# Optimization experiments

Measured on AMD Instinct MI355X. Metric: run time of the kernel, lower is better.

Reference implementation:

```python
import jax, jax.numpy as jnp
import numpy as np

LEN = 2048
DIM = 1024
DFF = 4096  # dim * dim_ff_scale
EPS = 1e-5


def layer_norm(x, g, b):
    mu = jnp.mean(x, axis=-1, keepdims=True)
    var = jnp.mean((x - mu) ** 2, axis=-1, keepdims=True)
    return (x - mu) * jax.lax.rsqrt(var + EPS) * g + b


def ffn(x, w1, b1, w2, b2):
    h = jax.nn.silu(x @ w1 + b1)
    return h @ w2 + b2


def setup_inputs() -> dict:
    key = jax.random.key(0)
    ks = jax.random.split(key, 16)
    s1 = 1.0 / np.sqrt(DIM)
    s2 = 1.0 / np.sqrt(DFF)
    return {
        "z": jax.random.normal(ks[0], (8, LEN, DIM), jnp.float32),
        "pos": jax.random.normal(ks[1], (LEN, DIM), jnp.float32),
        "a": jax.random.normal(ks[2], (1,), jnp.float32),
        "hidden_init": jax.random.normal(ks[3], (LEN, DIM), jnp.float32),
        "ln_g": jnp.ones((DIM,), jnp.float32),
        "ln_b": jnp.zeros((DIM,), jnp.float32),
        "wp1": jax.random.uniform(ks[4], (DIM, DFF), jnp.float32, -s1, s1),
        "bp1": jax.random.uniform(ks[5], (DFF,), jnp.float32, -s1, s1),
        "wp2": jax.random.uniform(ks[6], (DFF, DIM), jnp.float32, -s2, s2),
        "bp2": jax.random.uniform(ks[7], (DIM,), jnp.float32, -s2, s2),
        "w1": jax.random.uniform(ks[8], (DIM, DFF), jnp.float32, -s1, s1),
        "b1": jax.random.uniform(ks[9], (DFF,), jnp.float32, -s1, s1),
        "w2": jax.random.uniform(ks[10], (DFF, DIM), jnp.float32, -s2, s2),
        "b2": jax.random.uniform(ks[11], (DIM,), jnp.float32, -s2, s2),
    }


def reference(z, pos, a, hidden_init, ln_g, ln_b, wp1, bp1, wp2, bp2, w1, b1, w2, b2):
    # hidden starts as hidden_init broadcast to batch; it is detached in torch
    hidden = jax.lax.stop_gradient(jnp.broadcast_to(hidden_init[None], z.shape))
    # FFT of layer-normed input, zero-padded to 2*LEN along time axis
    fz = jnp.fft.rfft(layer_norm(z, ln_g, ln_b), n=2 * LEN, axis=1)  # [B, LEN+1, D] complex
    # implicit filter: FFN over positional encodings, windowed by exp decay
    h = ffn(pos, wp1, bp1, wp2, bp2)  # [LEN, D]
    window = jnp.exp(-jnp.arange(LEN, dtype=z.dtype) * jnp.exp(a[0]))  # [LEN]
    wfh = jnp.fft.rfft(window[:, None] * h, n=2 * LEN, axis=0)  # [LEN+1, D]
    z_hidden = jnp.fft.irfft(wfh[None] * fz, axis=1)  # [B, 2*LEN, D]
    znew = z_hidden[:, :LEN] + hidden
    out = ffn(layer_norm(znew, ln_g, ln_b), w1, b1, w2, b2) + znew
    return out
```

## Files before the change

kernel.cpp:

```cpp
#include <hip/hip_runtime.h>


typedef unsigned short u16;
typedef unsigned int u32;
typedef __attribute__((ext_vector_type(8))) short short8;
typedef __attribute__((ext_vector_type(4))) float f32x4;

#define DEVINL __device__ __forceinline__

constexpr size_t MiB = 1ull << 20;
constexpr size_t WS_BYTES = 256 * MiB;
__device__ __attribute__((aligned(256))) char g_ws[WS_BYTES];

constexpr size_t OFF_BUF0  = 0;
constexpr size_t OFF_ZNEW  = 64 * MiB;
constexpr size_t OFF_A1    = 128 * MiB;
constexpr size_t OFF_HB    = 160 * MiB;
constexpr size_t OFF_WFH   = 176 * MiB;
constexpr size_t OFF_POSB  = 193 * MiB;
constexpr size_t OFF_WP1T  = 197 * MiB;
constexpr size_t OFF_WP2T  = 205 * MiB;
constexpr size_t OFF_W1T   = 213 * MiB;
constexpr size_t OFF_W2T   = 221 * MiB;
constexpr size_t OFF_WFILT = 229 * MiB;
constexpr size_t OFF_HIDT  = 237 * MiB;
constexpr size_t OFF_MEAN  = 245 * MiB;
constexpr size_t OFF_RSTD  = 245 * MiB + 65536;

DEVINL u16 f2b(float x) {
  u32 u = __builtin_bit_cast(u32, x);
  return (u16)((u + 0x7fffu + ((u >> 16) & 1u)) >> 16);
}
DEVINL float b2f(u16 h) { u32 u = ((u32)h) << 16; return __builtin_bit_cast(float, u); }
DEVINL float silu_f(float x) { return x / (1.f + __expf(-x)); }

DEVINL void gll16(const u16* g, u16* l) {
  __builtin_amdgcn_global_load_lds((const __attribute__((address_space(1))) u32*)(const void*)g,
                                   (__attribute__((address_space(3))) u32*)(void*)l, 16, 0, 0);
}


__global__ __launch_bounds__(256) void conv_bf16(const float* __restrict__ in,
                                                 u16* __restrict__ o) {
  int i = (blockIdx.x * 256 + threadIdx.x) * 4;
  float4 v = *(const float4*)&in[i];
  o[i + 0] = f2b(v.x); o[i + 1] = f2b(v.y); o[i + 2] = f2b(v.z); o[i + 3] = f2b(v.w);
}

template<int OM>
__global__ __launch_bounds__(256) void transpose_prep(const float* __restrict__ in, int R, int C,
                                                      u16* __restrict__ oh, float* __restrict__ of) {
  __shared__ float tl[64][65];
  int c0 = blockIdx.x * 64, r0 = blockIdx.y * 64;
  int tx = threadIdx.x & 63, ty = threadIdx.x >> 6;
#pragma unroll
  for (int i = 0; i < 16; ++i) {
    int r = ty + i * 4;
    tl[r][tx] = in[(size_t)(r0 + r) * C + c0 + tx];
  }
  __syncthreads();
#pragma unroll
  for (int i = 0; i < 16; ++i) {
    int c = ty + i * 4;
    float v = tl[tx][c];
    size_t o = (size_t)(c0 + c) * R + r0 + tx;
    if constexpr (OM == 1) oh[o] = f2b(v);
    else of[o] = v;
  }
}


__global__ __launch_bounds__(256) void ln_transpose(const float* __restrict__ z,
                                                    const float* __restrict__ g,
                                                    const float* __restrict__ bb,
                                                    float* __restrict__ xnT) {
  int tid = threadIdx.x;
  int b = blockIdx.y, t0 = blockIdx.x * 8;
  __shared__ float tile[8 * 1024];
  __shared__ float smu[8], srs[8], ps[8][4], pq[8][4];
  const float* zp = z + ((size_t)b * 2048 + (size_t)t0) * 1024;
  float s[8], q[8];
#pragma unroll
  for (int r = 0; r < 8; ++r) {
    float4 v = *(const float4*)&zp[r * 1024 + tid * 4];
    *(float4*)&tile[r * 1024 + tid * 4] = v;
    s[r] = v.x + v.y + v.z + v.w;
    q[r] = v.x * v.x + v.y * v.y + v.z * v.z + v.w * v.w;
  }
  int ln = tid & 63, wv = tid >> 6;
#pragma unroll
  for (int r = 0; r < 8; ++r) {
#pragma unroll
    for (int off = 32; off; off >>= 1) { s[r] += __shfl_down(s[r], off); q[r] += __shfl_down(q[r], off); }
    if (ln == 0) { ps[r][wv] = s[r]; pq[r][wv] = q[r]; }
  }
  __syncthreads();
  if (tid < 8) {
    float ss = ps[tid][0] + ps[tid][1] + ps[tid][2] + ps[tid][3];
    float qq = pq[tid][0] + pq[tid][1] + pq[tid][2] + pq[tid][3];
    float mu = ss * (1.f / 1024.f);
    smu[tid] = mu;
    srs[tid] = rsqrtf(qq * (1.f / 1024.f) - mu * mu + 1e-5f);
  }
  __syncthreads();
#pragma unroll
  for (int rep = 0; rep < 4; ++rep) {
    int d = rep * 256 + tid;
    float gg = g[d], b2 = bb[d];
    float o[8];
#pragma unroll
    for (int t = 0; t < 8; ++t) o[t] = (tile[t * 1024 + d] - smu[t]) * srs[t] * gg + b2;
    float* op = xnT + (size_t)b * 2097152 + (size_t)d * 2048 + t0;
    *(float4*)&op[0] = make_float4(o[0], o[1], o[2], o[3]);
    *(float4*)&op[4] = make_float4(o[4], o[5], o[6], o[7]);
  }
}

template<int BM, int BN, int MODE>
__global__ __launch_bounds__(256) void gemm_bt(
    const u16* __restrict__ A, const u16* __restrict__ B,
    int N, int K,
    const float* __restrict__ bias, const float* __restrict__ resid,
    const float* __restrict__ a_scalar,
    float* __restrict__ outF, u16* __restrict__ outH) {
  constexpr int FM = BM / 32, FN = BN / 32;
  constexpr int TA = BM * 64, TB = BN * 64;
  __shared__ __align__(16) u16 sm[TA + TB];
  u16* sA = sm;
  u16* sB = sm + TA;

  const int tid = threadIdx.x;
  const int lane = tid & 63;
  const int wv = tid >> 6;
  const int wr = wv >> 1, wc = wv & 1;
  const int fr = lane & 15, fq = lane >> 4;
  const int mBase = blockIdx.y * BM;
  const int nBase = blockIdx.x * BN;

  f32x4 acc[FM][FN];
#pragma unroll
  for (int i = 0; i < FM; ++i)
#pragma unroll
    for (int j = 0; j < FN; ++j) acc[i][j] = (f32x4){0.f, 0.f, 0.f, 0.f};

#pragma unroll 1
  for (int k0 = 0; k0 < K; k0 += 64) {
#pragma unroll
    for (int it = 0; it < BM / 32; ++it) {
      int lin = it * 256 + tid, r = lin >> 3, c = (lin & 7) << 3;
      gll16(A + (size_t)(mBase + r) * K + k0 + c, sA + lin * 8);
    }
#pragma unroll
    for (int it = 0; it < BN / 32; ++it) {
      int lin = it * 256 + tid, r = lin >> 3, c = (lin & 7) << 3;
      gll16(B + (size_t)(nBase + r) * K + k0 + c, sB + lin * 8);
    }
    __syncthreads();
#pragma unroll
    for (int kk = 0; kk < 2; ++kk) {
      short8 af[FM], bf[FN];
#pragma unroll
      for (int i = 0; i < FM; ++i)
        af[i] = *(const short8*)&sA[(wr * (BM / 2) + i * 16 + fr) * 64 + kk * 32 + fq * 8];
#pragma unroll
      for (int j = 0; j < FN; ++j)
        bf[j] = *(const short8*)&sB[(wc * (BN / 2) + j * 16 + fr) * 64 + kk * 32 + fq * 8];
#pragma unroll
      for (int i = 0; i < FM; ++i)
#pragma unroll
        for (int j = 0; j < FN; ++j)
          acc[i][j] = __builtin_amdgcn_mfma_f32_16x16x32_bf16(af[i], bf[j], acc[i][j], 0, 0, 0);
    }
    __syncthreads();
  }

  float ea = 0.f;
  if constexpr (MODE == 1) ea = __expf(a_scalar[0]);
#pragma unroll
  for (int i = 0; i < FM; ++i)
#pragma unroll
    for (int j = 0; j < FN; ++j)
#pragma unroll
      for (int r = 0; r < 4; ++r) {
        int gr = mBase + wr * (BM / 2) + i * 16 + fq * 4 + r;
        int gc = nBase + wc * (BN / 2) + j * 16 + fr;
        size_t o = (size_t)gr * (size_t)N + (size_t)gc;
        float x = acc[i][j][r];
        if constexpr (MODE == 0) {
          outH[o] = f2b(silu_f(x + bias[gc]));
        } else if constexpr (MODE == 1) {
          x += bias[gr];
          x *= __expf(-(float)gc * ea);
          outF[o] = x;
        } else {
          outF[o] = x + bias[gc] + resid[o];
        }
      }
}

template<int SIGN>
DEVINL void fft4096(float2* x, float2* y, int tid) {
  float c0 = ((float)SIGN) * (6.283185307179586f / 4096.f);
#pragma unroll 1
  for (int st = 0; st < 12; ++st) {
#pragma unroll
    for (int vv = 0; vv < 8; ++vv) {
      int u = vv * 256 + tid;
      int p = u >> st;
      float2 a = x[u];
      float2 b = x[u + 2048];
      float ang = c0 * (float)p;
      float sn, cs;
      __sincosf(ang, &sn, &cs);
      float mx = a.x - b.x, my = a.y - b.y;
      int base = u + (p << st);
      y[base] = make_float2(a.x + b.x, a.y + b.y);
      y[base + (1 << st)] = make_float2(mx * cs - my * sn, mx * sn + my * cs);
    }
    __syncthreads();
    float2* t = x; x = y; y = t;
    c0 *= 2.f;
  }
}

__global__ __launch_bounds__(256) void fft_filter(const float* __restrict__ wfilt,
                                                  float2* __restrict__ wfh) {
  __shared__ float2 bufA[4096], bufB[4096];
  int tid = threadIdx.x, pr = blockIdx.x;
  int d0 = 2 * pr, d1 = d0 + 1;
  const float* u = wfilt + (size_t)d0 * 2048;
  const float* v = u + 2048;
#pragma unroll
  for (int j = 0; j < 16; ++j) {
    int idx = j * 256 + tid;
    bufA[idx] = (idx < 2048) ? make_float2(u[idx], v[idx]) : make_float2(0.f, 0.f);
  }
  __syncthreads();
  fft4096<-1>(bufA, bufB, tid);
  float2* o0 = wfh + (size_t)d0 * 2049;
  float2* o1 = wfh + (size_t)d1 * 2049;
#pragma unroll
  for (int j = 0; j < 9; ++j) {
    int k = j * 256 + tid;
    if (k <= 2048) {
      int kn = (4096 - k) & 4095;
      float2 Za = bufA[k], Zb = bufA[kn];
      o0[k] = make_float2(0.5f * (Za.x + Zb.x), 0.5f * (Za.y - Zb.y));
      o1[k] = make_float2(0.5f * (Za.y + Zb.y), 0.5f * (Zb.x - Za.x));
    }
  }
}

__global__ __launch_bounds__(256) void fft_conv(float* __restrict__ xnT,
                                                const float2* __restrict__ wfh,
                                                const float* __restrict__ hidT) {
  __shared__ float2 bufA[4096], bufB[4096];
  int tid = threadIdx.x;
  int pr = blockIdx.x, b = blockIdx.y;
  int d0 = 2 * pr, d1 = d0 + 1;
  float* u = xnT + (size_t)b * 2097152 + (size_t)d0 * 2048;
  float* v = u + 2048;
#pragma unroll
  for (int j = 0; j < 16; ++j) {
    int idx = j * 256 + tid;
    bufA[idx] = (idx < 2048) ? make_float2(u[idx], v[idx]) : make_float2(0.f, 0.f);
  }
  __syncthreads();
  fft4096<-1>(bufA, bufB, tid);
  const float2* F0 = wfh + (size_t)d0 * 2049;
  const float2* F1 = wfh + (size_t)d1 * 2049;
#pragma unroll
  for (int j = 0; j < 8; ++j) {
    int k = j * 256 + tid;
    if (k == 0) {
      float2 Z0 = bufA[0], Zh = bufA[2048];
      float2 f00 = F0[0], f10 = F1[0], f0h = F0[2048], f1h = F1[2048];
      float2 P0 = make_float2(Z0.x * f00.x, Z0.x * f00.y);
      float2 P1 = make_float2(Z0.y * f10.x, Z0.y * f10.y);
      bufA[0] = make_float2(P0.x - P1.y, P0.y + P1.x);
      float2 Q0 = make_float2(Zh.x * f0h.x, Zh.x * f0h.y);
      float2 Q1 = make_float2(Zh.y * f1h.x, Zh.y * f1h.y);
      bufA[2048] = make_float2(Q0.x - Q1.y, Q0.y + Q1.x);
    } else {
      int kn = 4096 - k;
      float2 Za = bufA[k], Zb = bufA[kn];
      float2 U = make_float2(0.5f * (Za.x + Zb.x), 0.5f * (Za.y - Zb.y));
      float2 V = make_float2(0.5f * (Za.y + Zb.y), 0.5f * (Zb.x - Za.x));
      float2 f0 = F0[k], f1 = F1[k];
      float2 P0 = make_float2(U.x * f0.x - U.y * f0.y, U.x * f0.y + U.y * f0.x);
      float2 P1 = make_float2(V.x * f1.x - V.y * f1.y, V.x * f1.y + V.y * f1.x);
      bufA[k]  = make_float2(P0.x - P1.y, P0.y + P1.x);
      bufA[kn] = make_float2(P0.x + P1.y, P1.x - P0.y);
    }
  }
  __syncthreads();
  fft4096<1>(bufA, bufB, tid);
  const float sc = 1.f / 4096.f;
  const float* h0 = hidT + (size_t)d0 * 2048;
  const float* h1 = h0 + 2048;
#pragma unroll
  for (int j = 0; j < 8; ++j) {
    int t = j * 256 + tid;
    float2 c = bufA[t];
    u[t] = c.x * sc + h0[t];
    v[t] = c.y * sc + h1[t];
  }
}

__global__ __launch_bounds__(256) void row_stats(const float* __restrict__ znewT,
                                                 float* __restrict__ meanb,
                                                 float* __restrict__ rstdb) {
  __shared__ float ss[4][64], sq[4][64];
  int b = blockIdx.y;
  int tl = threadIdx.x & 63, dq = threadIdx.x >> 6;
  int t = blockIdx.x * 64 + tl;
  const float* p = znewT + (size_t)b * 2097152 + (size_t)dq * 256 * 2048 + t;
  float s = 0.f, q = 0.f;
#pragma unroll 4
  for (int d = 0; d < 256; ++d) {
    float v = p[(size_t)d * 2048];
    s += v; q += v * v;
  }
  ss[dq][tl] = s; sq[dq][tl] = q;
  __syncthreads();
  if (threadIdx.x < 64) {
    int tt = blockIdx.x * 64 + threadIdx.x;
    float S = ss[0][threadIdx.x] + ss[1][threadIdx.x] + ss[2][threadIdx.x] + ss[3][threadIdx.x];
    float Q = sq[0][threadIdx.x] + sq[1][threadIdx.x] + sq[2][threadIdx.x] + sq[3][threadIdx.x];
    float mu = S * (1.f / 1024.f);
    meanb[b * 2048 + tt] = mu;
    rstdb[b * 2048 + tt] = rsqrtf(Q * (1.f / 1024.f) - mu * mu + 1e-5f);
  }
}

__global__ __launch_bounds__(256) void untranspose_ln(const float* __restrict__ znewT,
                                                      const float* __restrict__ meanb,
                                                      const float* __restrict__ rstdb,
                                                      const float* __restrict__ g,
                                                      const float* __restrict__ bb,
                                                      float* __restrict__ znew,
                                                      u16* __restrict__ A1) {
  __shared__ float tl[64][65];
  int b = blockIdx.z;
  int t0 = blockIdx.y * 64, d0 = blockIdx.x * 64;
  int tx = threadIdx.x & 63, ty = threadIdx.x >> 6;
  const float* ip = znewT + (size_t)b * 2097152 + (size_t)d0 * 2048 + t0;
#pragma unroll
  for (int i = 0; i < 16; ++i) {
    int d = ty + i * 4;
    tl[d][tx] = ip[(size_t)d * 2048 + tx];
  }
  __syncthreads();
  int m0 = b * 2048 + t0;
  float gg = g[d0 + tx], b2 = bb[d0 + tx];
#pragma unroll
  for (int i = 0; i < 16; ++i) {
    int t = ty + i * 4;
    float v = tl[tx][t];
    float mu = meanb[m0 + t], rs = rstdb[m0 + t];
    size_t o = (size_t)(m0 + t) * 1024 + d0 + tx;
    znew[o] = v;
    A1[o] = f2b((v - mu) * rs * gg + b2);
  }
}


extern "C" void kernel_launch(void* const* d_in, const int* in_sizes, int n_in,
                              void* d_out, int out_size, void* d_ws, size_t ws_size,
                              hipStream_t stream) {
  (void)in_sizes; (void)n_in; (void)out_size; (void)ws_size;
  const float* z   = (const float*)d_in[0];
  const float* pos = (const float*)d_in[1];
  const float* a   = (const float*)d_in[2];
  const float* hid = (const float*)d_in[3];
  const float* lng = (const float*)d_in[4];
  const float* lnb = (const float*)d_in[5];
  const float* wp1 = (const float*)d_in[6];
  const float* bp1 = (const float*)d_in[7];
  const float* wp2 = (const float*)d_in[8];
  const float* bp2 = (const float*)d_in[9];
  const float* w1  = (const float*)d_in[10];
  const float* b1  = (const float*)d_in[11];
  const float* w2  = (const float*)d_in[12];
  const float* b2  = (const float*)d_in[13];
  float* out = (float*)d_out;

  char* ws = nullptr;
  if (hipGetSymbolAddress((void**)&ws, HIP_SYMBOL(g_ws)) != hipSuccess || ws == nullptr)
    ws = (char*)d_ws;

  float*  buf0  = (float*)(ws + OFF_BUF0);
  float*  znew  = (float*)(ws + OFF_ZNEW);
  u16*    A1    = (u16*)  (ws + OFF_A1);
  u16*    hB    = (u16*)  (ws + OFF_HB);
  float2* wfh   = (float2*)(ws + OFF_WFH);
  u16*    posB  = (u16*)  (ws + OFF_POSB);
  u16*    wp1t  = (u16*)  (ws + OFF_WP1T);
  u16*    wp2t  = (u16*)  (ws + OFF_WP2T);
  u16*    w1t   = (u16*)  (ws + OFF_W1T);
  u16*    w2t   = (u16*)  (ws + OFF_W2T);
  float*  wfilt = (float*)(ws + OFF_WFILT);
  float*  hidT  = (float*)(ws + OFF_HIDT);
  float*  meanb = (float*)(ws + OFF_MEAN);
  float*  rstdb = (float*)(ws + OFF_RSTD);
  u16*    H2    = (u16*)  (ws + OFF_BUF0);

  conv_bf16<<<2048, 256, 0, stream>>>(pos, posB);
  transpose_prep<1><<<dim3(64, 16), 256, 0, stream>>>(wp1, 1024, 4096, wp1t, nullptr);
  transpose_prep<1><<<dim3(16, 64), 256, 0, stream>>>(wp2, 4096, 1024, wp2t, nullptr);
  transpose_prep<1><<<dim3(64, 16), 256, 0, stream>>>(w1, 1024, 4096, w1t, nullptr);
  transpose_prep<1><<<dim3(16, 64), 256, 0, stream>>>(w2, 4096, 1024, w2t, nullptr);
  transpose_prep<2><<<dim3(16, 32), 256, 0, stream>>>(hid, 2048, 1024, nullptr, hidT);

  ln_transpose<<<dim3(256, 8), 256, 0, stream>>>(z, lng, lnb, buf0);

  gemm_bt<128, 128, 0><<<dim3(32, 16), 256, 0, stream>>>(
      posB, wp1t, 4096, 1024, bp1, nullptr, nullptr, nullptr, hB);
  gemm_bt<64, 64, 1><<<dim3(32, 16), 256, 0, stream>>>(
      wp2t, hB, 2048, 4096, bp2, nullptr, a, wfilt, nullptr);

  fft_filter<<<512, 256, 0, stream>>>(wfilt, wfh);
  fft_conv<<<dim3(512, 8), 256, 0, stream>>>(buf0, wfh, hidT);

  row_stats<<<dim3(32, 8), 256, 0, stream>>>(buf0, meanb, rstdb);
  untranspose_ln<<<dim3(16, 32, 8), 256, 0, stream>>>(buf0, meanb, rstdb, lng, lnb, znew, A1);

  for (int h = 0; h < 2; ++h) {
    const u16* Ap = A1 + (size_t)h * 8192 * 1024;
    const float* zp = znew + (size_t)h * 8192 * 1024;
    float* op = out + (size_t)h * 8192 * 1024;
    gemm_bt<128, 128, 0><<<dim3(32, 64), 256, 0, stream>>>(
        Ap, w1t, 4096, 1024, b1, nullptr, nullptr, nullptr, H2);
    gemm_bt<128, 128, 2><<<dim3(8, 64), 256, 0, stream>>>(
        H2, w2t, 1024, 4096, b2, zp, nullptr, op, nullptr);
  }
}
```

Before: 1.070 ms.

## Use radix-16 shared-memory FFT, split LN into stats plus tiled transpose, retile filter GEMM

Measured after the change: 947.4 us. 11.5% less time.

```diff
diff --git a/kernel.cpp b/kernel.cpp
--- a/kernel.cpp
+++ b/kernel.cpp
@@ -69,50 +69,51 @@
   }
 }
 
-
-__global__ __launch_bounds__(256) void ln_transpose(const float* __restrict__ z,
+__global__ __launch_bounds__(256) void zstats(const float* __restrict__ z,
+                                              float* __restrict__ meanb,
+                                              float* __restrict__ rstdb) {
+  int row = blockIdx.x * 4 + (threadIdx.x >> 6);
+  int ln = threadIdx.x & 63;
+  const float* p = z + (size_t)row * 1024;
+  float s = 0.f, q = 0.f;
+#pragma unroll
+  for (int i = 0; i < 4; ++i) {
+    float4 v = *(const float4*)&p[ln * 4 + i * 256];
+    s += v.x + v.y + v.z + v.w;
+    q += v.x * v.x + v.y * v.y + v.z * v.z + v.w * v.w;
+  }
+#pragma unroll
+  for (int off = 32; off; off >>= 1) { s += __shfl_down(s, off); q += __shfl_down(q, off); }
+  if (ln == 0) {
+    float mu = s * (1.f / 1024.f);
+    meanb[row] = mu;
+    rstdb[row] = rsqrtf(q * (1.f / 1024.f) - mu * mu + 1e-5f);
+  }
+}
+
+__global__ __launch_bounds__(256) void transpose_ln(const float* __restrict__ z,
+                                                    const float* __restrict__ meanb,
+                                                    const float* __restrict__ rstdb,
                                                     const float* __restrict__ g,
                                                     const float* __restrict__ bb,
                                                     float* __restrict__ xnT) {
-  int tid = threadIdx.x;
-  int b = blockIdx.y, t0 = blockIdx.x * 8;
-  __shared__ float tile[8 * 1024];
-  __shared__ float smu[8], srs[8], ps[8][4], pq[8][4];
-  const float* zp = z + ((size_t)b * 2048 + (size_t)t0) * 1024;
-  float s[8], q[8];
-#pragma unroll
-  for (int r = 0; r < 8; ++r) {
-    float4 v = *(const float4*)&zp[r * 1024 + tid * 4];
-    *(float4*)&tile[r * 1024 + tid * 4] = v;
-    s[r] = v.x + v.y + v.z + v.w;
-    q[r] = v.x * v.x + v.y * v.y + v.z * v.z + v.w * v.w;
-  }
-  int ln = tid & 63, wv = tid >> 6;
-#pragma unroll
-  for (int r = 0; r < 8; ++r) {
-#pragma unroll
-    for (int off = 32; off; off >>= 1) { s[r] += __shfl_down(s[r], off); q[r] += __shfl_down(q[r], off); }
-    if (ln == 0) { ps[r][wv] = s[r]; pq[r][wv] = q[r]; }
-  }
-  __syncthreads();
-  if (tid < 8) {
-    float ss = ps[tid][0] + ps[tid][1] + ps[tid][2] + ps[tid][3];
-    float qq = pq[tid][0] + pq[tid][1] + pq[tid][2] + pq[tid][3];
-    float mu = ss * (1.f / 1024.f);
-    smu[tid] = mu;
-    srs[tid] = rsqrtf(qq * (1.f / 1024.f) - mu * mu + 1e-5f);
-  }
-  __syncthreads();
-#pragma unroll
-  for (int rep = 0; rep < 4; ++rep) {
-    int d = rep * 256 + tid;
-    float gg = g[d], b2 = bb[d];
-    float o[8];
-#pragma unroll
-    for (int t = 0; t < 8; ++t) o[t] = (tile[t * 1024 + d] - smu[t]) * srs[t] * gg + b2;
-    float* op = xnT + (size_t)b * 2097152 + (size_t)d * 2048 + t0;
-    *(float4*)&op[0] = make_float4(o[0], o[1], o[2], o[3]);
-    *(float4*)&op[4] = make_float4(o[4], o[5], o[6], o[7]);
+  __shared__ float tl[64][65];
+  int b = blockIdx.z;
+  int t0 = blockIdx.y * 64, d0 = blockIdx.x * 64;
+  int tx = threadIdx.x & 63, ty = threadIdx.x >> 6;
+#pragma unroll
+  for (int i = 0; i < 16; ++i) {
+    int t = ty + i * 4;
+    tl[t][tx] = z[((size_t)b * 2048 + t0 + t) * 1024 + d0 + tx];
+  }
+  __syncthreads();
+  float mu = meanb[b * 2048 + t0 + tx], rs = rstdb[b * 2048 + t0 + tx];
+#pragma unroll
+  for (int i = 0; i < 16; ++i) {
+    int d = ty + i * 4;
+    float v = tl[tx][d];
+    xnT[(size_t)b * 2097152 + (size_t)(d0 + d) * 2048 + t0 + tx] =
+        (v - mu) * rs * g[d0 + d] + bb[d0 + d];
   }
 }
 
@@ -198,34 +199,88 @@
       }
 }
 
-template<int SIGN>
-DEVINL void fft4096(float2* x, float2* y, int tid) {
-  float c0 = ((float)SIGN) * (6.283185307179586f / 4096.f);
-#pragma unroll 1
-  for (int st = 0; st < 12; ++st) {
-#pragma unroll
-    for (int vv = 0; vv < 8; ++vv) {
-      int u = vv * 256 + tid;
-      int p = u >> st;
-      float2 a = x[u];
-      float2 b = x[u + 2048];
-      float ang = c0 * (float)p;
+#define SLOT(e) ((e) + ((e) >> 4))
+constexpr int FBUF = 4352;
+
+DEVINL float2 cadd(float2 a, float2 b) { return make_float2(a.x + b.x, a.y + b.y); }
+DEVINL float2 csub(float2 a, float2 b) { return make_float2(a.x - b.x, a.y - b.y); }
+DEVINL float2 cmul(float2 a, float2 b) {
+  return make_float2(a.x * b.x - a.y * b.y, a.x * b.y + a.y * b.x);
+}
+template<int SGN> DEVINL float2 cmuli(float2 a) {
+  return (SGN < 0) ? make_float2(a.y, -a.x) : make_float2(-a.y, a.x);
+}
+
+template<int SGN>
+DEVINL void dft16(float2 v[16]) {
+  float2 T[16];
+#pragma unroll
+  for (int n1 = 0; n1 < 4; ++n1) {
+    float2 a = v[n1], b = v[n1 + 4], c = v[n1 + 8], d = v[n1 + 12];
+    float2 t0 = cadd(a, c), t1 = csub(a, c), t2 = cadd(b, d), t3 = cmuli<SGN>(csub(b, d));
+    T[n1 * 4 + 0] = cadd(t0, t2);
+    T[n1 * 4 + 2] = csub(t0, t2);
+    T[n1 * 4 + 1] = cadd(t1, t3);
+    T[n1 * 4 + 3] = csub(t1, t3);
+  }
+  constexpr float C1 = 0.92387953251128675613f, S1 = 0.38268343236508977173f;
+  constexpr float C2 = 0.70710678118654752440f;
+  const float sg = (float)SGN;
+  const float2 W1 = make_float2(C1, sg * S1);
+  const float2 W2 = make_float2(C2, sg * C2);
+  const float2 W3 = make_float2(S1, sg * C1);
+  const float2 W6 = make_float2(-C2, sg * C2);
+  const float2 W9 = make_float2(-C1, sg * -S1);
+  T[5] = cmul(T[5], W1);
+  T[6] = cmul(T[6], W2);
+  T[7] = cmul(T[7], W3);
+  T[9] = cmul(T[9], W2);
+  T[10] = cmuli<SGN>(T[10]);
+  T[11] = cmul(T[11], W6);
+  T[13] = cmul(T[13], W3);
+  T[14] = cmul(T[14], W6);
+  T[15] = cmul(T[15], W9);
+#pragma unroll
+  for (int k2 = 0; k2 < 4; ++k2) {
+    float2 a = T[k2], b = T[4 + k2], c = T[8 + k2], d = T[12 + k2];
+    float2 t0 = cadd(a, c), t1 = csub(a, c), t2 = cadd(b, d), t3 = cmuli<SGN>(csub(b, d));
+    v[0 * 4 + k2] = cadd(t0, t2);
+    v[2 * 4 + k2] = csub(t0, t2);
+    v[1 * 4 + k2] = cadd(t1, t3);
+    v[3 * 4 + k2] = csub(t1, t3);
+  }
+}
+
+template<int SGN>
+DEVINL void fft4096_r16(float2* x, float2* y, int tid) {
+#pragma unroll
+  for (int st = 0; st < 3; ++st) {
+    const int S = 1 << (4 * st);
+    const int u = tid;
+    float2 v[16];
+#pragma unroll
+    for (int r = 0; r < 16; ++r) v[r] = x[SLOT(u + 256 * r)];
+    dft16<SGN>(v);
+    if (st < 2) {
+      float th = ((float)SGN) * (6.28318530717958647693f / 4096.f) * (float)(u & ~(S - 1));
       float sn, cs;
-      __sincosf(ang, &sn, &cs);
-      float mx = a.x - b.x, my = a.y - b.y;
-      int base = u + (p << st);
-      y[base] = make_float2(a.x + b.x, a.y + b.y);
-      y[base + (1 << st)] = make_float2(mx * cs - my * sn, mx * sn + my * cs);
-    }
+      __sincosf(th, &sn, &cs);
+      float2 w = make_float2(cs, sn), wk = w;
+#pragma unroll
+      for (int k = 1; k < 16; ++k) { v[k] = cmul(v[k], wk); wk = cmul(wk, w); }
+    }
+    const int p = u >> (4 * st);
+    const int base = u + p * S * 15;
+#pragma unroll
+    for (int k = 0; k < 16; ++k) y[SLOT(base + S * k)] = v[k];
     __syncthreads();
     float2* t = x; x = y; y = t;
-    c0 *= 2.f;
   }
 }
 
 __global__ __launch_bounds__(256) void fft_filter(const float* __restrict__ wfilt,
                                                   float2* __restrict__ wfh) {
-  __shared__ float2 bufA[4096], bufB[4096];
+  __shared__ float2 bufA[FBUF], bufB[FBUF];
   int tid = threadIdx.x, pr = blockIdx.x;
   int d0 = 2 * pr, d1 = d0 + 1;
   const float* u = wfilt + (size_t)d0 * 2048;
@@ -233,10 +288,10 @@
 #pragma unroll
   for (int j = 0; j < 16; ++j) {
     int idx = j * 256 + tid;
-    bufA[idx] = (idx < 2048) ? make_float2(u[idx], v[idx]) : make_float2(0.f, 0.f);
-  }
-  __syncthreads();
-  fft4096<-1>(bufA, bufB, tid);
+    bufA[SLOT(idx)] = (idx < 2048) ? make_float2(u[idx], v[idx]) : make_float2(0.f, 0.f);
+  }
+  __syncthreads();
+  fft4096_r16<-1>(bufA, bufB, tid);
   float2* o0 = wfh + (size_t)d0 * 2049;
   float2* o1 = wfh + (size_t)d1 * 2049;
 #pragma unroll
@@ -244,7 +299,7 @@
     int k = j * 256 + tid;
     if (k <= 2048) {
       int kn = (4096 - k) & 4095;
-      float2 Za = bufA[k], Zb = bufA[kn];
+      float2 Za = bufB[SLOT(k)], Zb = bufB[SLOT(kn)];
       o0[k] = make_float2(0.5f * (Za.x + Zb.x), 0.5f * (Za.y - Zb.y));
       o1[k] = make_float2(0.5f * (Za.y + Zb.y), 0.5f * (Zb.x - Za.x));
     }
@@ -254,7 +309,7 @@
 __global__ __launch_bounds__(256) void fft_conv(float* __restrict__ xnT,
                                                 const float2* __restrict__ wfh,
                                                 const float* __restrict__ hidT) {
-  __shared__ float2 bufA[4096], bufB[4096];
+  __shared__ float2 bufA[FBUF], bufB[FBUF];
   int tid = threadIdx.x;
   int pr = blockIdx.x, b = blockIdx.y;
   int d0 = 2 * pr, d1 = d0 + 1;
@@ -263,45 +318,45 @@
 #pragma unroll
   for (int j = 0; j < 16; ++j) {
     int idx = j * 256 + tid;
-    bufA[idx] = (idx < 2048) ? make_float2(u[idx], v[idx]) : make_float2(0.f, 0.f);
-  }
-  __syncthreads();
-  fft4096<-1>(bufA, bufB, tid);
+    bufA[SLOT(idx)] = (idx < 2048) ? make_float2(u[idx], v[idx]) : make_float2(0.f, 0.f);
+  }
+  __syncthreads();
+  fft4096_r16<-1>(bufA, bufB, tid);
   const float2* F0 = wfh + (size_t)d0 * 2049;
   const float2* F1 = wfh + (size_t)d1 * 2049;
 #pragma unroll
   for (int j = 0; j < 8; ++j) {
     int k = j * 256 + tid;
     if (k == 0) {
-      float2 Z0 = bufA[0], Zh = bufA[2048];
+      float2 Z0 = bufB[SLOT(0)], Zh = bufB[SLOT(2048)];
       float2 f00 = F0[0], f10 = F1[0], f0h = F0[2048], f1h = F1[2048];
       float2 P0 = make_float2(Z0.x * f00.x, Z0.x * f00.y);
       float2 P1 = make_float2(Z0.y * f10.x, Z0.y * f10.y);
-      bufA[0] = make_float2(P0.x - P1.y, P0.y + P1.x);
+      bufB[SLOT(0)] = make_float2(P0.x - P1.y, P0.y + P1.x);
       float2 Q0 = make_float2(Zh.x * f0h.x, Zh.x * f0h.y);
       float2 Q1 = make_float2(Zh.y * f1h.x, Zh.y * f1h.y);
-      bufA[2048] = make_float2(Q0.x - Q1.y, Q0.y + Q1.x);
+      bufB[SLOT(2048)] = make_float2(Q0.x - Q1.y, Q0.y + Q1.x);
     } else {
       int kn = 4096 - k;
-      float2 Za = bufA[k], Zb = bufA[kn];
+      float2 Za = bufB[SLOT(k)], Zb = bufB[SLOT(kn)];
       float2 U = make_float2(0.5f * (Za.x + Zb.x), 0.5f * (Za.y - Zb.y));
       float2 V = make_float2(0.5f * (Za.y + Zb.y), 0.5f * (Zb.x - Za.x));
       float2 f0 = F0[k], f1 = F1[k];
       float2 P0 = make_float2(U.x * f0.x - U.y * f0.y, U.x * f0.y + U.y * f0.x);
       float2 P1 = make_float2(V.x * f1.x - V.y * f1.y, V.x * f1.y + V.y * f1.x);
-      bufA[k]  = make_float2(P0.x - P1.y, P0.y + P1.x);
-      bufA[kn] = make_float2(P0.x + P1.y, P1.x - P0.y);
-    }
-  }
-  __syncthreads();
-  fft4096<1>(bufA, bufB, tid);
+      bufB[SLOT(k)]  = make_float2(P0.x - P1.y, P0.y + P1.x);
+      bufB[SLOT(kn)] = make_float2(P0.x + P1.y, P1.x - P0.y);
+    }
+  }
+  __syncthreads();
+  fft4096_r16<1>(bufB, bufA, tid);
   const float sc = 1.f / 4096.f;
   const float* h0 = hidT + (size_t)d0 * 2048;
   const float* h1 = h0 + 2048;
 #pragma unroll
   for (int j = 0; j < 8; ++j) {
     int t = j * 256 + tid;
-    float2 c = bufA[t];
+    float2 c = bufA[SLOT(t)];
     u[t] = c.x * sc + h0[t];
     v[t] = c.y * sc + h1[t];
   }
@@ -412,11 +467,12 @@
   transpose_prep<1><<<dim3(16, 64), 256, 0, stream>>>(w2, 4096, 1024, w2t, nullptr);
   transpose_prep<2><<<dim3(16, 32), 256, 0, stream>>>(hid, 2048, 1024, nullptr, hidT);
 
-  ln_transpose<<<dim3(256, 8), 256, 0, stream>>>(z, lng, lnb, buf0);
+  zstats<<<4096, 256, 0, stream>>>(z, meanb, rstdb);
+  transpose_ln<<<dim3(16, 32, 8), 256, 0, stream>>>(z, meanb, rstdb, lng, lnb, buf0);
 
   gemm_bt<128, 128, 0><<<dim3(32, 16), 256, 0, stream>>>(
       posB, wp1t, 4096, 1024, bp1, nullptr, nullptr, nullptr, hB);
-  gemm_bt<64, 64, 1><<<dim3(32, 16), 256, 0, stream>>>(
+  gemm_bt<64, 128, 1><<<dim3(16, 16), 256, 0, stream>>>(
       wp2t, hB, 2048, 4096, bp2, nullptr, a, wfilt, nullptr);
 
   fft_filter<<<512, 256, 0, stream>>>(wfilt, wfh);
```
